# Optimization experiments

Measured on AMD Instinct MI355X. Metric: run time of the kernel, lower is better.

The kernel has to match this reference:

```python
import jax, jax.numpy as jnp
import numpy as np

VOCAB = 32000
EMB = 200
HID = 128
B = 64
T = 64


def setup_inputs() -> dict:
    key = jax.random.key(0)
    ks = jax.random.split(key, 10)
    s = 0.05
    return {
        "tokens": jax.random.randint(ks[0], (B, T), 0, VOCAB, dtype=jnp.int32),
        "emb": jax.random.normal(ks[1], (VOCAB, EMB), jnp.float32) * s,
        "W0": jax.random.normal(ks[2], (EMB, 4 * HID), jnp.float32) * s,
        "U0": jax.random.normal(ks[3], (HID, 4 * HID), jnp.float32) * s,
        "b0": jax.random.normal(ks[4], (4 * HID,), jnp.float32) * s,
        "W1": jax.random.normal(ks[5], (HID, 4 * HID), jnp.float32) * s,
        "U1": jax.random.normal(ks[6], (HID, 4 * HID), jnp.float32) * s,
        "b1": jax.random.normal(ks[7], (4 * HID,), jnp.float32) * s,
        "Wout": jax.random.normal(ks[8], (HID, VOCAB), jnp.float32) * s,
        "bout": jax.random.normal(ks[9], (VOCAB,), jnp.float32) * s,
    }


def _lstm_cell(x, h, c, W, U, b):
    # Keras LSTMCell gate order: i, f, g(candidate), o
    z = x @ W + h @ U + b  # [B, 4H]
    i, f, g, o = jnp.split(z, 4, axis=-1)
    c_new = jax.nn.sigmoid(f) * c + jax.nn.sigmoid(i) * jnp.tanh(g)
    h_new = jax.nn.sigmoid(o) * jnp.tanh(c_new)
    return h_new, c_new


def reference(tokens, emb, W0, U0, b0, W1, U1, b1, Wout, bout):
    x = emb[tokens]                      # [B, T, EMB]
    xt = jnp.transpose(x, (1, 0, 2))     # time-major [T, B, EMB]
    zeros = jnp.zeros((tokens.shape[0], HID), x.dtype)
    init = (zeros, zeros, zeros, zeros)  # h0, c0, h1, c1

    def step(carry, xw):
        h0, c0, h1, c1 = carry
        h0, c0 = _lstm_cell(xw, h0, c0, W0, U0, b0)
        h1, c1 = _lstm_cell(h0, h1, c1, W1, U1, b1)
        out = jax.nn.relu(h1 @ Wout + bout)  # [B, VOCAB]
        return (h0, c0, h1, c1), out

    _, outs = jax.lax.scan(step, init, xt)   # [T, B, VOCAB]
    return jnp.transpose(outs, (1, 0, 2))    # [B, T, VOCAB]
```

## Files before the change

### kernel.cpp

```cpp
#include <hip/hip_runtime.h>
#include <stdint.h>
#include <stddef.h>

typedef _Float16 f16;
typedef _Float16 f16x2 __attribute__((ext_vector_type(2)));
typedef _Float16 f16x8 __attribute__((ext_vector_type(8)));
typedef float    f32x4 __attribute__((ext_vector_type(4)));

#define VOCAB 32000
#define EMBD  200
#define HID   128
#define NB    64
#define NT    64
#define G4    (4*HID)

__device__ __forceinline__ float sigf(float x) {
    return __builtin_amdgcn_rcpf(1.f + __expf(-x));
}
__device__ __forceinline__ float tanhf_(float x) {
    return 1.f - 2.f * __builtin_amdgcn_rcpf(1.f + __expf(2.f * x));
}

__global__ __launch_bounds__(256) void prep_rec(
    const float* __restrict__ U0, const float* __restrict__ W1,
    const float* __restrict__ U1, uint32_t* __restrict__ wp) {
    int idx = blockIdx.x * 256 + threadIdx.x;
    if (idx >= 3 * 64 * G4) return;
    int m = idx >> 15;
    int rem = idx & 32767;
    int p = rem >> 9, j = rem & 511;
    const float* W = (m == 0) ? U0 : (m == 1) ? W1 : U1;
    f16x2 v;
    v[0] = (f16)W[(2 * p) * G4 + j];
    v[1] = (f16)W[(2 * p + 1) * G4 + j];
    ((f16x2*)wp)[idx] = v;
}

__global__ __launch_bounds__(256) void prep_woutT(
    const float* __restrict__ Wout, f16* __restrict__ WoutT) {
    __shared__ __align__(16) f16 tile[64 * 136];
    const int n0 = blockIdx.x * 64;
    const int t = threadIdx.x;
    for (int i = t; i < 64 * 128; i += 256) {
        int k = i >> 6, n = i & 63;
        tile[n * 136 + k] = (f16)Wout[(size_t)k * VOCAB + n0 + n];
    }
    __syncthreads();
    for (int i = t; i < 1024; i += 256) {
        int n = i >> 4, u = i & 15;
        *(uint4*)(WoutT + (size_t)(n0 + n) * HID + u * 8) =
            *(const uint4*)&tile[n * 136 + u * 8];
    }
}

__global__ __launch_bounds__(256) void embed_w0(
    const int* __restrict__ tokens, const float* __restrict__ emb,
    const float* __restrict__ W0, const float* __restrict__ b0,
    float* __restrict__ z0) {
    __shared__ __align__(16) float xs[EMBD * 16];
    __shared__ int tok[16];
    const int t = threadIdx.x, blk = blockIdx.x;
    if (t < 16) tok[t] = tokens[blk * 16 + t];
    __syncthreads();
    for (int i = t; i < EMBD * 16; i += 256) {
        int r = i / EMBD, k = i - r * EMBD;
        xs[k * 16 + r] = emb[(size_t)tok[r] * EMBD + k];
    }
    __syncthreads();
    const int j = t * 2;
    f32x4 accA[4], accB[4];
#pragma unroll
    for (int grp = 0; grp < 4; ++grp) {
        accA[grp] = f32x4{0.f, 0.f, 0.f, 0.f};
        accB[grp] = f32x4{0.f, 0.f, 0.f, 0.f};
    }
    for (int k = 0; k < EMBD; ++k) {
        float2 w = *(const float2*)(W0 + (size_t)k * G4 + j);
        const f32x4* xv = (const f32x4*)(xs + k * 16);
#pragma unroll
        for (int grp = 0; grp < 4; ++grp) {
            f32x4 x = xv[grp];
            accA[grp] += x * w.x;
            accB[grp] += x * w.y;
        }
    }
    float bx = b0[j], by = b0[j + 1];
#pragma unroll
    for (int grp = 0; grp < 4; ++grp)
#pragma unroll
        for (int r = 0; r < 4; ++r) {
            int row = blk * 16 + grp * 4 + r;
            float2 o; o.x = accA[grp][r] + bx; o.y = accB[grp][r] + by;
            *(float2*)(z0 + (size_t)row * G4 + j) = o;
        }
}

__global__ __launch_bounds__(512, 1) void lstm_scan(
    const float* __restrict__ z0base, const uint32_t* __restrict__ wp,
    const float* __restrict__ b1, f16* __restrict__ H1) {
    const int b = blockIdx.x, t = threadIdx.x;
    const int g = t >> 7, q = t & 127, jb = q << 2;
    __shared__ __align__(16) float zpart[4][G4];
    __shared__ __align__(16) f16 h0s[HID];
    __shared__ __align__(16) f16 h1s[HID];

    const f16x8* wp8 = (const f16x8*)wp;
    f16x2 wu0[64], ww1[64], wu1[64];
    const int wbase = (g * 16) * 128 + q;
#pragma unroll
    for (int kk = 0; kk < 16; ++kk) {
        *(f16x8*)&wu0[kk * 4] = wp8[0 * 8192 + wbase + kk * 128];
        *(f16x8*)&ww1[kk * 4] = wp8[1 * 8192 + wbase + kk * 128];
        *(f16x8*)&wu1[kk * 4] = wp8[2 * 8192 + wbase + kk * 128];
    }
    float b1a = 0.f, b1b = 0.f, b1c = 0.f, b1d = 0.f;
    if (t < HID) {
        b1a = b1[t]; b1b = b1[t + 128]; b1c = b1[t + 256]; b1d = b1[t + 384];
        h0s[t] = (f16)0.f; h1s[t] = (f16)0.f;
    }
    float c0 = 0.f, c1 = 0.f;
    __syncthreads();

    const float* zb = z0base + (size_t)b * NT * G4;
    f16* hout = H1 + (size_t)b * NT * HID;

    for (int step = 0; step < NT; ++step) {
        float za = 0.f, zbv = 0.f, zc = 0.f, zd = 0.f;
        if (t < HID) {
            const float* zr = zb + (size_t)step * G4 + t;
            za = zr[0]; zbv = zr[128]; zc = zr[256]; zd = zr[384];
        }
        float a0 = 0.f, a1 = 0.f, a2 = 0.f, a3 = 0.f;
        {
            f16x2 hh[16];
            const f16x8* hp = (const f16x8*)h0s + g * 4;
            *(f16x8*)&hh[0] = hp[0]; *(f16x8*)&hh[4] = hp[1];
            *(f16x8*)&hh[8] = hp[2]; *(f16x8*)&hh[12] = hp[3];
#pragma unroll
            for (int kk = 0; kk < 16; ++kk) {
                f16x2 h = hh[kk];
                a0 = __builtin_amdgcn_fdot2(wu0[kk * 4 + 0], h, a0, false);
                a1 = __builtin_amdgcn_fdot2(wu0[kk * 4 + 1], h, a1, false);
                a2 = __builtin_amdgcn_fdot2(wu0[kk * 4 + 2], h, a2, false);
                a3 = __builtin_amdgcn_fdot2(wu0[kk * 4 + 3], h, a3, false);
            }
        }
        *(f32x4*)&zpart[g][jb] = f32x4{a0, a1, a2, a3};
        __syncthreads();
        if (t < HID) {
            float zi = za  + zpart[0][t]       + zpart[1][t]       + zpart[2][t]       + zpart[3][t];
            float zf = zbv + zpart[0][t + 128] + zpart[1][t + 128] + zpart[2][t + 128] + zpart[3][t + 128];
            float zg = zc  + zpart[0][t + 256] + zpart[1][t + 256] + zpart[2][t + 256] + zpart[3][t + 256];
            float zo = zd  + zpart[0][t + 384] + zpart[1][t + 384] + zpart[2][t + 384] + zpart[3][t + 384];
            c0 = sigf(zf) * c0 + sigf(zi) * tanhf_(zg);
            h0s[t] = (f16)(sigf(zo) * tanhf_(c0));
        }
        __syncthreads();
        a0 = 0.f; a1 = 0.f; a2 = 0.f; a3 = 0.f;
        {
            f16x2 hh[16];
            const f16x8* hp0 = (const f16x8*)h0s + g * 4;
            *(f16x8*)&hh[0] = hp0[0]; *(f16x8*)&hh[4] = hp0[1];
            *(f16x8*)&hh[8] = hp0[2]; *(f16x8*)&hh[12] = hp0[3];
#pragma unroll
            for (int kk = 0; kk < 16; ++kk) {
                f16x2 h = hh[kk];
                a0 = __builtin_amdgcn_fdot2(ww1[kk * 4 + 0], h, a0, false);
                a1 = __builtin_amdgcn_fdot2(ww1[kk * 4 + 1], h, a1, false);
                a2 = __builtin_amdgcn_fdot2(ww1[kk * 4 + 2], h, a2, false);
                a3 = __builtin_amdgcn_fdot2(ww1[kk * 4 + 3], h, a3, false);
            }
            const f16x8* hp1 = (const f16x8*)h1s + g * 4;
            *(f16x8*)&hh[0] = hp1[0]; *(f16x8*)&hh[4] = hp1[1];
            *(f16x8*)&hh[8] = hp1[2]; *(f16x8*)&hh[12] = hp1[3];
#pragma unroll
            for (int kk = 0; kk < 16; ++kk) {
                f16x2 h = hh[kk];
                a0 = __builtin_amdgcn_fdot2(wu1[kk * 4 + 0], h, a0, false);
                a1 = __builtin_amdgcn_fdot2(wu1[kk * 4 + 1], h, a1, false);
                a2 = __builtin_amdgcn_fdot2(wu1[kk * 4 + 2], h, a2, false);
                a3 = __builtin_amdgcn_fdot2(wu1[kk * 4 + 3], h, a3, false);
            }
        }
        *(f32x4*)&zpart[g][jb] = f32x4{a0, a1, a2, a3};
        __syncthreads();
        if (t < HID) {
            float zi = b1a + zpart[0][t]       + zpart[1][t]       + zpart[2][t]       + zpart[3][t];
            float zf = b1b + zpart[0][t + 128] + zpart[1][t + 128] + zpart[2][t + 128] + zpart[3][t + 128];
            float zg = b1c + zpart[0][t + 256] + zpart[1][t + 256] + zpart[2][t + 256] + zpart[3][t + 256];
            float zo = b1d + zpart[0][t + 384] + zpart[1][t + 384] + zpart[2][t + 384] + zpart[3][t + 384];
            c1 = sigf(zf) * c1 + sigf(zi) * tanhf_(zg);
            float h1v = sigf(zo) * tanhf_(c1);
            h1s[t] = (f16)h1v;
            hout[step * HID + t] = (f16)h1v;
        }
        __syncthreads();
    }
}

__global__ __launch_bounds__(256) void out_gemm(
    const f16* __restrict__ H1, const f16* __restrict__ WT,
    const float* __restrict__ bout, float* __restrict__ out) {
    __shared__ __align__(16) f16 Asub[128 * 128];
    __shared__ __align__(16) f16 Bsub[128 * 128];
    const int n0 = blockIdx.x * 128;
    const int m0 = blockIdx.y * 128;
    const int t = threadIdx.x;

    const uint4* Ag = (const uint4*)(H1 + (size_t)m0 * HID);
    const uint4* Bg = (const uint4*)(WT + (size_t)n0 * HID);
#pragma unroll
    for (int i = 0; i < 8; ++i) {
        int Gr = i * 256 + t;
        int row = Gr >> 4, gg = Gr & 15;
        int d = (row << 4) | (gg ^ (row & 7));
        ((uint4*)Asub)[d] = Ag[Gr];
        ((uint4*)Bsub)[d] = Bg[Gr];
    }
    __syncthreads();

    const int w = t >> 6, l = t & 63;
    const int wm = (w >> 1) * 64, wn = (w & 1) * 64;
    const int lr = l & 15, lk = l >> 4;
    f32x4 zero = {0.f, 0.f, 0.f, 0.f};
    f32x4 acc[4][4];
#pragma unroll
    for (int mi = 0; mi < 4; ++mi)
#pragma unroll
        for (int ni = 0; ni < 4; ++ni) acc[mi][ni] = zero;

#pragma unroll
    for (int kc = 0; kc < 4; ++kc) {
        f16x8 af[4], bf[4];
#pragma unroll
        for (int mi = 0; mi < 4; ++mi) {
            int row = wm + mi * 16 + lr;
            int gg = kc * 4 + lk;
            af[mi] = *(const f16x8*)&Asub[(row << 7) + ((gg ^ (row & 7)) << 3)];
        }
#pragma unroll
        for (int ni = 0; ni < 4; ++ni) {
            int row = wn + ni * 16 + lr;
            int gg = kc * 4 + lk;
            bf[ni] = *(const f16x8*)&Bsub[(row << 7) + ((gg ^ (row & 7)) << 3)];
        }
#pragma unroll
        for (int mi = 0; mi < 4; ++mi)
#pragma unroll
            for (int ni = 0; ni < 4; ++ni)
                acc[mi][ni] = __builtin_amdgcn_mfma_f32_16x16x32_f16(
                    af[mi], bf[ni], acc[mi][ni], 0, 0, 0);
    }

#pragma unroll
    for (int ni = 0; ni < 4; ++ni) {
        int n = n0 + wn + ni * 16 + lr;
        float bv = bout[n];
#pragma unroll
        for (int mi = 0; mi < 4; ++mi) {
            int mrow = m0 + wm + mi * 16 + lk * 4;
#pragma unroll
            for (int r = 0; r < 4; ++r) {
                float v = acc[mi][ni][r] + bv;
                __builtin_nontemporal_store(v > 0.f ? v : 0.f,
                                            &out[(size_t)(mrow + r) * VOCAB + n]);
            }
        }
    }
}

extern "C" void kernel_launch(void* const* d_in, const int* in_sizes, int n_in,
                              void* d_out, int out_size, void* d_ws, size_t ws_size,
                              hipStream_t stream) {
    const int*   tokens = (const int*)d_in[0];
    const float* emb  = (const float*)d_in[1];
    const float* W0   = (const float*)d_in[2];
    const float* U0   = (const float*)d_in[3];
    const float* b0   = (const float*)d_in[4];
    const float* W1   = (const float*)d_in[5];
    const float* U1   = (const float*)d_in[6];
    const float* b1   = (const float*)d_in[7];
    const float* Wout = (const float*)d_in[8];
    const float* bout = (const float*)d_in[9];
    float* out = (float*)d_out;

    char* ws = (char*)d_ws;
    float*    z0base = (float*)ws;
    f16*      WoutT  = (f16*)ws;
    uint32_t* wp     = (uint32_t*)(ws + 8388608);
    f16*      H1     = (f16*)(ws + 8781824);

    embed_w0  <<<256, 256, 0, stream>>>(tokens, emb, W0, b0, z0base);
    prep_rec  <<<384, 256, 0, stream>>>(U0, W1, U1, wp);
    lstm_scan <<<64, 512, 0, stream>>>(z0base, wp, b1, H1);
    prep_woutT<<<500, 256, 0, stream>>>(Wout, WoutT);
    out_gemm  <<<dim3(250, 32), 256, 0, stream>>>(H1, WoutT, bout, out);
}
```

Baseline: 292.0 us.

## Merge prep kernels, overlap Wout transpose with LSTM scan, stage output stores

```diff
diff --git a/kernel.cpp b/kernel.cpp
--- a/kernel.cpp
+++ b/kernel.cpp
@@ -21,45 +21,28 @@
     return 1.f - 2.f * __builtin_amdgcn_rcpf(1.f + __expf(2.f * x));
 }
 
-__global__ __launch_bounds__(256) void prep_rec(
-    const float* __restrict__ U0, const float* __restrict__ W1,
-    const float* __restrict__ U1, uint32_t* __restrict__ wp) {
-    int idx = blockIdx.x * 256 + threadIdx.x;
-    if (idx >= 3 * 64 * G4) return;
-    int m = idx >> 15;
-    int rem = idx & 32767;
-    int p = rem >> 9, j = rem & 511;
-    const float* W = (m == 0) ? U0 : (m == 1) ? W1 : U1;
-    f16x2 v;
-    v[0] = (f16)W[(2 * p) * G4 + j];
-    v[1] = (f16)W[(2 * p + 1) * G4 + j];
-    ((f16x2*)wp)[idx] = v;
-}
-
-__global__ __launch_bounds__(256) void prep_woutT(
-    const float* __restrict__ Wout, f16* __restrict__ WoutT) {
-    __shared__ __align__(16) f16 tile[64 * 136];
-    const int n0 = blockIdx.x * 64;
-    const int t = threadIdx.x;
-    for (int i = t; i < 64 * 128; i += 256) {
-        int k = i >> 6, n = i & 63;
-        tile[n * 136 + k] = (f16)Wout[(size_t)k * VOCAB + n0 + n];
-    }
-    __syncthreads();
-    for (int i = t; i < 1024; i += 256) {
-        int n = i >> 4, u = i & 15;
-        *(uint4*)(WoutT + (size_t)(n0 + n) * HID + u * 8) =
-            *(const uint4*)&tile[n * 136 + u * 8];
-    }
-}
-
-__global__ __launch_bounds__(256) void embed_w0(
+__global__ __launch_bounds__(256) void fused_prep(
     const int* __restrict__ tokens, const float* __restrict__ emb,
     const float* __restrict__ W0, const float* __restrict__ b0,
-    float* __restrict__ z0) {
+    const float* __restrict__ U0, const float* __restrict__ W1,
+    const float* __restrict__ U1,
+    float* __restrict__ z0, uint32_t* __restrict__ wp) {
+    const int t = threadIdx.x;
+    if (blockIdx.x >= 256) {
+        int idx = (blockIdx.x - 256) * 256 + t;
+        int m = idx >> 15;
+        int rem = idx & 32767;
+        int p = rem >> 9, j = rem & 511;
+        const float* W = (m == 0) ? U0 : (m == 1) ? W1 : U1;
+        f16x2 v;
+        v[0] = (f16)W[(2 * p) * G4 + j];
+        v[1] = (f16)W[(2 * p + 1) * G4 + j];
+        ((f16x2*)wp)[idx] = v;
+        return;
+    }
     __shared__ __align__(16) float xs[EMBD * 16];
     __shared__ int tok[16];
-    const int t = threadIdx.x, blk = blockIdx.x;
+    const int blk = blockIdx.x;
     if (t < 16) tok[t] = tokens[blk * 16 + t];
     __syncthreads();
     for (int i = t; i < EMBD * 16; i += 256) {
@@ -95,10 +78,28 @@
         }
 }
 
-__global__ __launch_bounds__(512, 1) void lstm_scan(
+__global__ __launch_bounds__(512, 1) void scan_fused(
     const float* __restrict__ z0base, const uint32_t* __restrict__ wp,
-    const float* __restrict__ b1, f16* __restrict__ H1) {
-    const int b = blockIdx.x, t = threadIdx.x;
+    const float* __restrict__ b1, f16* __restrict__ H1,
+    const float* __restrict__ Wout, f16* __restrict__ WoutT, int do_wt) {
+    const int t = threadIdx.x;
+    if (blockIdx.x >= 64) {
+        if (!do_wt) return;
+        __shared__ __align__(16) f16 tile[64 * 136];
+        const int n0 = (blockIdx.x - 64) * 64;
+        for (int i = t; i < 64 * 128; i += 512) {
+            int k = i >> 6, n = i & 63;
+            tile[n * 136 + k] = (f16)Wout[(size_t)k * VOCAB + n0 + n];
+        }
+        __syncthreads();
+        for (int i = t; i < 1024; i += 512) {
+            int n = i >> 4, u = i & 15;
+            *(uint4*)(WoutT + (size_t)(n0 + n) * HID + u * 8) =
+                *(const uint4*)&tile[n * 136 + u * 8];
+        }
+        return;
+    }
+    const int b = blockIdx.x;
     const int g = t >> 7, q = t & 127, jb = q << 2;
     __shared__ __align__(16) float zpart[4][G4];
     __shared__ __align__(16) f16 h0s[HID];
@@ -198,13 +199,31 @@
     }
 }
 
+__global__ __launch_bounds__(256) void prep_woutT(
+    const float* __restrict__ Wout, f16* __restrict__ WoutT) {
+    __shared__ __align__(16) f16 tile[64 * 136];
+    const int n0 = blockIdx.x * 64;
+    const int t = threadIdx.x;
+    for (int i = t; i < 64 * 128; i += 256) {
+        int k = i >> 6, n = i & 63;
+        tile[n * 136 + k] = (f16)Wout[(size_t)k * VOCAB + n0 + n];
+    }
+    __syncthreads();
+    for (int i = t; i < 1024; i += 256) {
+        int n = i >> 4, u = i & 15;
+        *(uint4*)(WoutT + (size_t)(n0 + n) * HID + u * 8) =
+            *(const uint4*)&tile[n * 136 + u * 8];
+    }
+}
+
 __global__ __launch_bounds__(256) void out_gemm(
     const f16* __restrict__ H1, const f16* __restrict__ WT,
     const float* __restrict__ bout, float* __restrict__ out) {
-    __shared__ __align__(16) f16 Asub[128 * 128];
-    __shared__ __align__(16) f16 Bsub[128 * 128];
-    const int n0 = blockIdx.x * 128;
-    const int m0 = blockIdx.y * 128;
+    __shared__ __align__(16) char lraw[128 * 132 * 4];
+    f16* Asub = (f16*)lraw;
+    f16* Bsub = (f16*)(lraw + 32768);
+    const int m0 = blockIdx.x * 128;
+    const int n0 = blockIdx.y * 128;
     const int t = threadIdx.x;
 
     const uint4* Ag = (const uint4*)(H1 + (size_t)m0 * HID);
@@ -252,20 +271,34 @@
                     af[mi], bf[ni], acc[mi][ni], 0, 0, 0);
     }
 
-#pragma unroll
-    for (int ni = 0; ni < 4; ++ni) {
-        int n = n0 + wn + ni * 16 + lr;
-        float bv = bout[n];
-#pragma unroll
-        for (int mi = 0; mi < 4; ++mi) {
-            int mrow = m0 + wm + mi * 16 + lk * 4;
-#pragma unroll
-            for (int r = 0; r < 4; ++r) {
-                float v = acc[mi][ni][r] + bv;
-                __builtin_nontemporal_store(v > 0.f ? v : 0.f,
-                                            &out[(size_t)(mrow + r) * VOCAB + n]);
-            }
-        }
+    __syncthreads();
+    float* ldsf = (float*)lraw;
+#pragma unroll
+    for (int mi = 0; mi < 4; ++mi) {
+        int lrow = wm + mi * 16 + lk * 4;
+#pragma unroll
+        for (int ni = 0; ni < 4; ++ni) {
+            int lcol = wn + ni * 16 + lr;
+#pragma unroll
+            for (int r = 0; r < 4; ++r)
+                ldsf[(lrow + r) * 132 + lcol] = acc[mi][ni][r];
+        }
+    }
+    __syncthreads();
+    const int col = (t * 4) & 127;
+    const int rbase = t >> 5;
+    float4 bv = *(const float4*)&bout[n0 + col];
+#pragma unroll
+    for (int c = 0; c < 16; ++c) {
+        int row = c * 8 + rbase;
+        float4 v = *(const float4*)&ldsf[row * 132 + col];
+        float4 o;
+        o.x = v.x + bv.x; o.y = v.y + bv.y; o.z = v.z + bv.z; o.w = v.w + bv.w;
+        o.x = o.x > 0.f ? o.x : 0.f;
+        o.y = o.y > 0.f ? o.y : 0.f;
+        o.z = o.z > 0.f ? o.z : 0.f;
+        o.w = o.w > 0.f ? o.w : 0.f;
+        *(float4*)&out[(size_t)(m0 + row) * VOCAB + n0 + col] = o;
     }
 }
 
@@ -286,13 +319,15 @@
 
     char* ws = (char*)d_ws;
     float*    z0base = (float*)ws;
-    f16*      WoutT  = (f16*)ws;
     uint32_t* wp     = (uint32_t*)(ws + 8388608);
     f16*      H1     = (f16*)(ws + 8781824);
-
-    embed_w0  <<<256, 256, 0, stream>>>(tokens, emb, W0, b0, z0base);
-    prep_rec  <<<384, 256, 0, stream>>>(U0, W1, U1, wp);
-    lstm_scan <<<64, 512, 0, stream>>>(z0base, wp, b1, H1);
-    prep_woutT<<<500, 256, 0, stream>>>(Wout, WoutT);
-    out_gemm  <<<dim3(250, 32), 256, 0, stream>>>(H1, WoutT, bout, out);
-}
+    const bool big_ws = ws_size >= (size_t)18100000;
+    f16*      WoutT  = big_ws ? (f16*)(ws + 9830400) : (f16*)ws;
+
+    fused_prep<<<640, 256, 0, stream>>>(tokens, emb, W0, b0, U0, W1, U1, z0base, wp);
+    scan_fused<<<564, 512, 0, stream>>>(z0base, wp, b1, H1, Wout, WoutT,
+                                        big_ws ? 1 : 0);
+    if (!big_ws)
+        prep_woutT<<<500, 256, 0, stream>>>(Wout, WoutT);
+    out_gemm<<<dim3(32, 250), 256, 0, stream>>>(H1, WoutT, bout, out);
+}
```

New measurement: 274.4 us. 1.06x faster.
